# Kernel optimization log

Measured on AMD Instinct MI355X. Metric: run time of the kernel, lower is better.

The kernel has to match this reference:

```python
import jax, jax.numpy as jnp
import numpy as np

N, Cin, H, W = 8, 256, 32, 32
Cout, K = 512, 3
DK, DV, NH = 128, 128, 8
DKH, DVH = DK // NH, DV // NH
HW = H * W


def conv2d(x, w, b, stride, pad):
    y = jax.lax.conv_general_dilated(
        x, w, (stride, stride), [(pad, pad), (pad, pad)],
        dimension_numbers=("NCHW", "OIHW", "NCHW"))
    return y + b[None, :, None, None]


def rel_to_abs(x):
    # x: (B, Nh*, L, 2L-1) -> (B, Nh*, L, L) via pad/reshape trick
    B, Nh, L, _ = x.shape
    x = jnp.concatenate([x, jnp.zeros((B, Nh, L, 1), x.dtype)], axis=3)
    flat = x.reshape(B, Nh, L * 2 * L)
    flat = jnp.concatenate([flat, jnp.zeros((B, Nh, L - 1), x.dtype)], axis=2)
    return flat.reshape(B, Nh, L + 1, 2 * L - 1)[:, :, :L, L - 1:]


def relative_logits_1d(q, rel_k, Hq, Wq, case):
    # q: (N, Nh, Hq, Wq, dkh); rel_k: (2*Wq-1, dkh)
    rl = jnp.einsum('bhxyd,md->bhxym', q, rel_k)             # (N,Nh,Hq,Wq,2Wq-1)
    rl = rel_to_abs(rl.reshape(-1, NH * Hq, Wq, 2 * Wq - 1))  # (N,Nh*Hq,Wq,Wq)
    rl = rl.reshape(-1, NH, Hq, Wq, Wq)[:, :, :, None]        # (N,Nh,Hq,1,Wq,Wq)
    rl = jnp.broadcast_to(rl, (rl.shape[0], NH, Hq, Hq, Wq, Wq))  # axes (b,h,x,i,y,j)
    if case == 'w':
        rl = rl.transpose(0, 1, 2, 4, 3, 5)   # (b,h,x,y,i,j)
    else:  # 'h'
        rl = rl.transpose(0, 1, 4, 2, 5, 3)   # (b,h,y,x,j,i)
    return rl.reshape(-1, NH, HW, HW)


def setup_inputs() -> dict:
    key = jax.random.key(0)
    ks = jax.random.split(key, 9)
    s = 0.05
    return {
        'x': jax.random.normal(ks[0], (N, Cin, H, W), jnp.float32),
        'w_out': jax.random.normal(ks[1], (Cout - DV, Cin, K, K), jnp.float32) * s,
        'b_out': jnp.zeros((Cout - DV,), jnp.float32),
        'w_kqv': jax.random.normal(ks[2], (2 * DK + DV, Cin, 1, 1), jnp.float32) * s,
        'b_kqv': jnp.zeros((2 * DK + DV,), jnp.float32),
        'w_attn': jax.random.normal(ks[3], (DV, DV, 1, 1), jnp.float32) * s,
        'b_attn': jnp.zeros((DV,), jnp.float32),
        'key_rel_w': jax.random.normal(ks[4], (2 * W - 1, DKH), jnp.float32),
        'key_rel_h': jax.random.normal(ks[5], (2 * H - 1, DKH), jnp.float32),
    }


def reference(x, w_out, b_out, w_kqv, b_kqv, w_attn, b_attn, key_rel_w, key_rel_h):
    conv_out = conv2d(x, w_out, b_out, 1, (K - 1) // 2)       # (N, Cout-DV, H, W)
    kqv = conv2d(x, w_kqv, b_kqv, 1, 0)                       # (N, 2DK+DV, H, W)
    k, q, v = jnp.split(kqv, [DK, 2 * DK], axis=1)
    q = q * (DKH ** -0.5)
    q5 = q.reshape(N, NH, DKH, H, W)
    flat_q = q5.reshape(N, NH, DKH, HW)
    flat_k = k.reshape(N, NH, DKH, HW)
    flat_v = v.reshape(N, NH, DVH, HW)
    logits = jnp.einsum('bhdm,bhdn->bhmn', flat_q, flat_k)    # (N,NH,HW,HW)
    qt = q5.transpose(0, 1, 3, 4, 2)                          # (N,NH,H,W,dkh)
    rl_w = relative_logits_1d(qt, key_rel_w, H, W, 'w')
    rl_h = relative_logits_1d(qt.transpose(0, 1, 3, 2, 4), key_rel_h, W, H, 'h')
    logits = logits + rl_h + rl_w
    weights = jax.nn.softmax(logits, axis=-1)
    attn = jnp.einsum('bhmn,bhdn->bhmd', weights, flat_v)     # (N,NH,HW,DVH)
    # faithful to torch: raw reshape (N,NH,HW,DVH)->(N,NH,DVH,H,W)->(N,DV,H,W)
    attn = attn.reshape(N, DV, H, W)
    attn = conv2d(attn, w_attn, b_attn, 1, 0)
    return jnp.concatenate([conv_out, attn], axis=1)
```

## Files before the change

### kernel.cpp

```cpp
#include <hip/hip_runtime.h>
#include <hip/hip_bf16.h>


typedef short v8s __attribute__((ext_vector_type(8)));
typedef float v4f __attribute__((ext_vector_type(4)));

#define WB2_US   0u
#define WK2_US   884736u
#define WA2_US   983040u
#define KRWB_US  999424u
#define KRHB_US  1000448u
#define XC_US    1001472u
#define ART2_US  3368960u

#define KS_US    0u
#define QS_US    1048576u
#define VTS_US   2097152u
#define ART1_US  7340032u

#define QSCALE 0.360673760f
#define SHIFT2 17.3123405f

__device__ __forceinline__ unsigned short f2bs(float f) {
  __hip_bfloat16 h = __float2bfloat16(f);
  return *reinterpret_cast<unsigned short*>(&h);
}

__global__ __launch_bounds__(256) void prep_kernel(
    const float* __restrict__ w_out, const float* __restrict__ w_kqv,
    const float* __restrict__ w_attn, const float* __restrict__ krw,
    const float* __restrict__ krh, unsigned short* __restrict__ ws) {
  int i = blockIdx.x * 256 + threadIdx.x;
  if (i < 884736) {
    int j = i & 7, l = (i >> 3) & 63;
    int r = i >> 9;
    int tap = r % 9; int r2 = r / 9;
    int kc = r2 & 7, nt = (r2 >> 3) & 3, coG = r2 >> 5;
    int co = coG * 64 + nt * 16 + (l & 15);
    int ci = kc * 32 + (l >> 4) * 8 + j;
    ws[WB2_US + i] = f2bs(w_out[(size_t)co * 2304 + ci * 9 + tap]);
  } else if (i < 983040) {
    int o = i - 884736;
    int j = o & 7, l = (o >> 3) & 63, kc = (o >> 9) & 7, nt = (o >> 12) & 3;
    int coG = o >> 14;
    int co = coG * 64 + nt * 16 + (l & 15);
    int ci = kc * 32 + (l >> 4) * 8 + j;
    ws[WK2_US + o] = f2bs(w_kqv[co * 256 + ci]);
  } else if (i < 999424) {
    int o = i - 983040;
    int j = o & 7, l = (o >> 3) & 63, kc = (o >> 9) & 3, nt = (o >> 11) & 3;
    int coG = o >> 13;
    int co = coG * 64 + nt * 16 + (l & 15);
    int ci = kc * 32 + (l >> 4) * 8 + j;
    ws[WA2_US + o] = f2bs(w_attn[co * 128 + ci]);
  } else if (i < 1000448) {
    int j = i - 999424; int c = j >> 4, d = j & 15;
    ws[KRWB_US + j] = (c < 63) ? f2bs(krw[c * 16 + d]) : (unsigned short)0;
  } else if (i < 1001472) {
    int j = i - 1000448; int c = j >> 4, d = j & 15;
    ws[KRHB_US + j] = (c < 63) ? f2bs(krh[c * 16 + d]) : (unsigned short)0;
  }
}

__global__ __launch_bounds__(256) void zero_xc_kernel(unsigned short* __restrict__ xc) {
  int i = blockIdx.x * 256 + threadIdx.x;
  uint4 z = {0u, 0u, 0u, 0u};
  ((uint4*)xc)[i] = z;
}

__global__ __launch_bounds__(256) void xt_kernel(
    const float* __restrict__ x, unsigned short* __restrict__ xc) {
  __shared__ float t[64][65];
  int tid = threadIdx.x; int pl = tid & 63, cg = tid >> 6;
  int pos0 = blockIdx.x * 64, ci0 = blockIdx.y * 64, b = blockIdx.z;
  const float* xb = x + ((size_t)(b * 256 + ci0)) * 1024 + pos0;
#pragma unroll
  for (int i = 0; i < 16; ++i) {
    int ci_l = cg * 16 + i;
    t[ci_l][pl] = xb[(size_t)ci_l * 1024 + pl];
  }
  __syncthreads();
#pragma unroll
  for (int i = 0; i < 16; ++i) {
    int pos_l = cg * 16 + i;
    int pos = pos0 + pos_l;
    int y = (pos >> 5) + 1, xx = (pos & 31) + 1;
    int ci = ci0 + pl;
    xc[((size_t)((b * 8 + (ci >> 5)) * 34 + y) * 34 + xx) * 32 + (ci & 31)] =
        f2bs(t[pl][pos_l]);
  }
}

__global__ __launch_bounds__(256) void kqv_mfma(
    const unsigned short* __restrict__ xc, const unsigned short* __restrict__ wk2,
    const float* __restrict__ bkqv, unsigned short* __restrict__ dq) {
  int tid = threadIdx.x;
  int lane = tid & 63; int il = lane & 15, q = lane >> 4;
  int wv = tid >> 6; int mh = wv >> 1, nh = wv & 1;
  int m0 = blockIdx.x * 64, coG = blockIdx.y;
  int b = m0 >> 10, pos0 = m0 & 1023;
  int row0 = pos0 >> 5;
  v4f acc[2][2];
#pragma unroll
  for (int mi = 0; mi < 2; ++mi)
#pragma unroll
    for (int ni = 0; ni < 2; ++ni) acc[mi][ni] = (v4f){0.f, 0.f, 0.f, 0.f};

  int pix[2];
#pragma unroll
  for (int mi = 0; mi < 2; ++mi)
    pix[mi] = (row0 + mh + 1) * 34 + (mi * 16 + il + 1);
  const unsigned short* bt = wk2 + (size_t)coG * 16384 + lane * 8;
  const unsigned short* at = xc + (size_t)(b * 8) * 36992 + q * 8;

  v8s afS[4][2], bfS[4][2];
#pragma unroll
  for (int p = 0; p < 3; ++p) {
#pragma unroll
    for (int ni = 0; ni < 2; ++ni)
      bfS[p][ni] = *(const v8s*)(bt + ((nh * 2 + ni) * 8 + p) * 512);
#pragma unroll
    for (int mi = 0; mi < 2; ++mi)
      afS[p][mi] = *(const v8s*)(at + (size_t)p * 36992 + pix[mi] * 32);
  }

#pragma unroll
  for (int kc = 0; kc < 8; ++kc) {
    if (kc + 3 < 8) {
      int kn = kc + 3, s = kn & 3;
#pragma unroll
      for (int ni = 0; ni < 2; ++ni)
        bfS[s][ni] = *(const v8s*)(bt + ((nh * 2 + ni) * 8 + kn) * 512);
#pragma unroll
      for (int mi = 0; mi < 2; ++mi)
        afS[s][mi] = *(const v8s*)(at + (size_t)kn * 36992 + pix[mi] * 32);
    }
    int cs = kc & 3;
#pragma unroll
    for (int mi = 0; mi < 2; ++mi)
#pragma unroll
      for (int ni = 0; ni < 2; ++ni)
        acc[mi][ni] = __builtin_amdgcn_mfma_f32_16x16x32_bf16(
            afS[cs][mi], bfS[cs][ni], acc[mi][ni], 0, 0, 0);
  }
  int co0 = coG * 64;
#pragma unroll
  for (int ni = 0; ni < 2; ++ni) {
    int nt = nh * 2 + ni;
    int cob = co0 + nt * 16;
    int co = cob + il;
    float bias = bkqv[co];
    int cls = cob >> 7;
    int h = (cob >> 4) & 7;
    size_t bh = (size_t)(b * 8 + h);
#pragma unroll
    for (int mi = 0; mi < 2; ++mi) {
      int mt = mh * 2 + mi;
      int pos = pos0 + mt * 16 + q * 4;
      v4f a = acc[mi][ni];
#pragma unroll
      for (int r = 0; r < 4; ++r) {
        float v = a[r] + bias;
        int p = pos + r;
        if (cls == 0)      dq[KS_US + bh * 16384 + p * 16 + il] = f2bs(v);
        else if (cls == 1) dq[QS_US + bh * 16384 + p * 16 + il] = f2bs(v * QSCALE);
        else               dq[VTS_US + bh * 16384 + ((p >> 5) * 16 + il) * 32 + (p & 31)] = f2bs(v);
      }
    }
  }
}

__global__ __launch_bounds__(256) void attn_mfma(
    unsigned short* __restrict__ dq, const unsigned short* __restrict__ krwb,
    const unsigned short* __restrict__ krhb, unsigned short* __restrict__ wsart) {
  __shared__ float lds[4][2448];
  int tid = threadIdx.x; int w = tid >> 6, lane = tid & 63;
  int il = lane & 15, q = lane >> 4;
  int bh = blockIdx.y; int b = bh >> 3, h = bh & 7;
  int m0 = blockIdx.x * 64 + w * 16;
  int my = m0 >> 5, mxb = m0 & 31;
  float* pw = lds[w];
  float* ph = pw + 1024;
  unsigned short* pl = (unsigned short*)(ph + 1088);

  const v8s z8 = {0, 0, 0, 0, 0, 0, 0, 0};
  const v4f z4 = {0.f, 0.f, 0.f, 0.f};

  const unsigned short* qrow = dq + QS_US + (size_t)bh * 16384 + (m0 + il) * 16;
  v8s qa = *(const v8s*)(qrow + (q & 1) * 8);
  qa = (q < 2) ? qa : z8;

#pragma unroll
  for (int nt = 0; nt < 4; ++nt) {
    int c = nt * 16 + il;
    v8s bw = *(const v8s*)(krwb + c * 16 + (q & 1) * 8);
    v8s bhh = *(const v8s*)(krhb + c * 16 + (q & 1) * 8);
    bw = (q < 2) ? bw : z8;
    bhh = (q < 2) ? bhh : z8;
    v4f pwc = __builtin_amdgcn_mfma_f32_16x16x32_bf16(qa, bw, z4, 0, 0, 0);
    v4f phc = __builtin_amdgcn_mfma_f32_16x16x32_bf16(qa, bhh, z4, 0, 0, 0);
#pragma unroll
    for (int r = 0; r < 4; ++r) {
      pw[(q * 4 + r) * 64 + c] = pwc[r];
      ph[(q * 4 + r) * 68 + c] = phc[r] - SHIFT2;
    }
  }
  __builtin_amdgcn_wave_barrier();

  float pwv[2][4];
#pragma unroll
  for (int nt2 = 0; nt2 < 2; ++nt2)
#pragma unroll
    for (int r = 0; r < 4; ++r)
      pwv[nt2][r] = pw[il * 64 + (nt2 * 16 + q * 4 + r) - mxb - il + 31];

  v4f oacc = z4;
  float sacc = 0.f;
  const unsigned short* kbase = dq + KS_US + (size_t)bh * 16384;
  const unsigned short* vbase = dq + VTS_US + (size_t)bh * 16384;

  v8s kb0 = *(const v8s*)(kbase + (il) * 16 + (q & 1) * 8);
  v8s kb1 = *(const v8s*)(kbase + (16 + il) * 16 + (q & 1) * 8);
  v8s vb0 = *(const v8s*)(vbase + (il) * 32 + q * 8);

  for (int ny = 0; ny < 32; ++ny) {
    v8s kc0 = (q < 2) ? kb0 : z8;
    v8s kc1 = (q < 2) ? kb1 : z8;
    v8s vcur = vb0;
    if (ny < 31) {
      kb0 = *(const v8s*)(kbase + ((ny + 1) * 32 + il) * 16 + (q & 1) * 8);
      kb1 = *(const v8s*)(kbase + ((ny + 1) * 32 + 16 + il) * 16 + (q & 1) * 8);
      vb0 = *(const v8s*)(vbase + ((ny + 1) * 16 + il) * 32 + q * 8);
    }
    float phv = ph[il * 68 + (ny - my + 31)];
    v4f s[2];
    s[0] = __builtin_amdgcn_mfma_f32_16x16x32_bf16(kc0, qa, z4, 0, 0, 0);
    s[1] = __builtin_amdgcn_mfma_f32_16x16x32_bf16(kc1, qa, z4, 0, 0, 0);
#pragma unroll
    for (int nt2 = 0; nt2 < 2; ++nt2) {
      float p[4];
#pragma unroll
      for (int r = 0; r < 4; ++r) {
        float t = s[nt2][r] + pwv[nt2][r] + phv;
        p[r] = exp2f(t);
        sacc += p[r];
      }
      uint2 pk;
      pk.x = (unsigned)f2bs(p[0]) | ((unsigned)f2bs(p[1]) << 16);
      pk.y = (unsigned)f2bs(p[2]) | ((unsigned)f2bs(p[3]) << 16);
      *(uint2*)(pl + il * 40 + nt2 * 16 + q * 4) = pk;
    }
    __builtin_amdgcn_wave_barrier();
    v8s pf = *(const v8s*)(pl + il * 40 + q * 8);
    oacc = __builtin_amdgcn_mfma_f32_16x16x32_bf16(pf, vcur, oacc, 0, 0, 0);
    __builtin_amdgcn_wave_barrier();
  }

  sacc += __shfl_xor(sacc, 16);
  sacc += __shfl_xor(sacc, 32);

  unsigned short* abase = (b < 6) ? (dq + ART1_US + (size_t)b * 131072)
                                  : (wsart + (size_t)(b - 6) * 131072);
#pragma unroll
  for (int r = 0; r < 4; ++r) {
    float sr = __shfl(sacc, q * 4 + r);
    int m = m0 + q * 4 + r;
    int c = h * 16 + (m >> 6);
    int pp = (m & 63) * 16 + il;
    abase[((c >> 5) * 1024 + pp) * 32 + (c & 31)] = f2bs(oacc[r] / sr);
  }
}

__global__ __launch_bounds__(256) void attn_out_mfma(
    const unsigned short* __restrict__ dq, const unsigned short* __restrict__ wsart,
    const unsigned short* __restrict__ wa2, const float* __restrict__ ba,
    float* __restrict__ out) {
  int tid = threadIdx.x;
  int lane = tid & 63; int il = lane & 15, q = lane >> 4;
  int wv = tid >> 6; int mh = wv >> 1, nh = wv & 1;
  int m0 = blockIdx.x * 64, coG = blockIdx.y;
  int b = m0 >> 10, pp0 = m0 & 1023;
  const unsigned short* ab = (b < 6) ? (dq + ART1_US + (size_t)b * 131072)
                                     : (wsart + (size_t)(b - 6) * 131072);
  const unsigned short* bt = wa2 + (size_t)coG * 8192 + lane * 8;
  v4f acc[2][2];
#pragma unroll
  for (int mi = 0; mi < 2; ++mi)
#pragma unroll
    for (int ni = 0; ni < 2; ++ni) acc[mi][ni] = (v4f){0.f, 0.f, 0.f, 0.f};
#pragma unroll
  for (int kc = 0; kc < 4; ++kc) {
    v8s af[2], bf[2];
#pragma unroll
    for (int ni = 0; ni < 2; ++ni)
      bf[ni] = *(const v8s*)(bt + ((nh * 2 + ni) * 4 + kc) * 512);
#pragma unroll
    for (int mi = 0; mi < 2; ++mi)
      af[mi] = *(const v8s*)(ab + (kc * 1024 + pp0 + (mh * 2 + mi) * 16 + il) * 32 + q * 8);
#pragma unroll
    for (int mi = 0; mi < 2; ++mi)
#pragma unroll
      for (int ni = 0; ni < 2; ++ni)
        acc[mi][ni] = __builtin_amdgcn_mfma_f32_16x16x32_bf16(
            af[mi], bf[ni], acc[mi][ni], 0, 0, 0);
  }
  int co0 = coG * 64;
#pragma unroll
  for (int ni = 0; ni < 2; ++ni) {
    int co = co0 + (nh * 2 + ni) * 16 + il;
    float bias = ba[co];
#pragma unroll
    for (int mi = 0; mi < 2; ++mi) {
      int mt = mh * 2 + mi;
      v4f a = acc[mi][ni];
      float4 v; v.x = a[0] + bias; v.y = a[1] + bias;
      v.z = a[2] + bias; v.w = a[3] + bias;
      *(float4*)(out + ((size_t)(b * 512 + 384 + co)) * 1024 + pp0 + mt * 16 + q * 4) = v;
    }
  }
}

__global__ __launch_bounds__(256, 2) void conv_mfma(
    const unsigned short* __restrict__ xc, const unsigned short* __restrict__ wb3,
    const float* __restrict__ bo, float* __restrict__ out) {
  __shared__ unsigned short xcs[2][4608];
  int tid = threadIdx.x;
  int lane = tid & 63; int il = lane & 15, q = lane >> 4;
  int wv = tid >> 6; int mh = wv >> 1, nh = wv & 1;
  int bx = blockIdx.x, nset = blockIdx.y;
  int b = bx & 7, pt = bx >> 3;
  int pos0 = pt * 64, y0 = pt * 2;
  const unsigned short* xb = xc + ((size_t)(b * 8) * 1156 + y0 * 34) * 32;

  v4f acc[2][3];
#pragma unroll
  for (int mi = 0; mi < 2; ++mi)
#pragma unroll
    for (int j = 0; j < 3; ++j) acc[mi][j] = (v4f){0.f, 0.f, 0.f, 0.f};

  const unsigned short* wp[3];
#pragma unroll
  for (int j = 0; j < 3; ++j) {
    int nfg = nset * 6 + nh * 3 + j;
    int coG = nfg >> 2, nt = nfg & 3;
    wp[j] = wb3 + (size_t)(coG * 4 + nt) * 36864 + lane * 8;
  }

  auto stageX = [&](int buf, int kc) {
    const unsigned short* src = xb + (size_t)kc * 36992;
#pragma unroll
    for (int t = 0; t < 3; ++t) {
      int s = wv + t * 4;
      if (s < 9) {
        int C = s * 64 + lane;
        int row = C / 136, rem = C % 136;
        int qv = rem / 34, xx = rem % 34;
        const unsigned short* g = src + ((row * 136 + xx * 4 + qv) << 3);
        __builtin_amdgcn_global_load_lds(
            (const __attribute__((address_space(1))) void*)g,
            (__attribute__((address_space(3))) void*)(&xcs[buf][s * 512]),
            16, 0, 0);
      }
    }
  };

  stageX(0, 0);
  v8s bS[5][3];
#pragma unroll
  for (int p = 0; p < 4; ++p)
#pragma unroll
    for (int j = 0; j < 3; ++j)
      bS[p][j] = *(const v8s*)(wp[j] + (size_t)p * 512);
  __syncthreads();

#pragma unroll
  for (int kc = 0; kc < 8; ++kc) {
    int buf = kc & 1;
    if (kc < 7) stageX(buf ^ 1, kc + 1);
#pragma unroll
    for (int tap = 0; tap < 9; ++tap) {
      int it = kc * 9 + tap;
      if (it + 4 < 72) {
#pragma unroll
        for (int j = 0; j < 3; ++j)
          bS[(it + 4) % 5][j] = *(const v8s*)(wp[j] + (size_t)(it + 4) * 512);
      }
      int ky = tap / 3, kx = tap % 3;
      v8s af[2];
#pragma unroll
      for (int mi = 0; mi < 2; ++mi)
        af[mi] = *(const v8s*)&xcs[buf][((mh + ky) * 4 + q) * 272 +
                                        (mi * 16 + kx + il) * 8];
#pragma unroll
      for (int mi = 0; mi < 2; ++mi)
#pragma unroll
        for (int j = 0; j < 3; ++j)
          acc[mi][j] = __builtin_amdgcn_mfma_f32_16x16x32_bf16(
              af[mi], bS[it % 5][j], acc[mi][j], 0, 0, 0);
    }
    __syncthreads();
  }

  int co0 = nset * 96;
#pragma unroll
  for (int j = 0; j < 3; ++j) {
    int co = co0 + (nh * 3 + j) * 16 + il;
    float bias = bo[co];
#pragma unroll
    for (int mi = 0; mi < 2; ++mi) {
      v4f a = acc[mi][j];
      float4 v; v.x = a[0] + bias; v.y = a[1] + bias;
      v.z = a[2] + bias; v.w = a[3] + bias;
      *(float4*)(out + ((size_t)(b * 512 + co)) * 1024 +
                 pos0 + mh * 32 + mi * 16 + q * 4) = v;
    }
  }
}

extern "C" void kernel_launch(void* const* d_in, const int* in_sizes, int n_in,
                              void* d_out, int out_size, void* d_ws, size_t ws_size,
                              hipStream_t stream) {
  const float* x      = (const float*)d_in[0];
  const float* b_out  = (const float*)d_in[2];
  const float* b_kqv  = (const float*)d_in[4];
  const float* b_attn = (const float*)d_in[6];
  const float* krw    = (const float*)d_in[7];
  const float* krh    = (const float*)d_in[8];
  unsigned short* ws = (unsigned short*)d_ws;
  float* out = (float*)d_out;
  unsigned short* dq = (unsigned short*)d_out;

  prep_kernel<<<3912, 256, 0, stream>>>(
      (const float*)d_in[1], (const float*)d_in[3], (const float*)d_in[5],
      krw, krh, ws);
  zero_xc_kernel<<<1156, 256, 0, stream>>>(ws + XC_US);
  xt_kernel<<<dim3(16, 4, 8), 256, 0, stream>>>(x, ws + XC_US);
  kqv_mfma<<<dim3(128, 6), 256, 0, stream>>>(
      ws + XC_US, ws + WK2_US, b_kqv, dq);
  attn_mfma<<<dim3(16, 64), 256, 0, stream>>>(
      dq, ws + KRWB_US, ws + KRHB_US, ws + ART2_US);
  attn_out_mfma<<<dim3(128, 2), 256, 0, stream>>>(
      dq, ws + ART2_US, ws + WA2_US, b_attn, out);
  conv_mfma<<<dim3(128, 4), 256, 0, stream>>>(
      ws + XC_US, ws + WB2_US, b_out, out);
}
```

Measured before the change: 159.3 us.

## Stage conv weights in LDS and double block tile to 512 threads

The 3x3 conv kernel now uses 512-thread blocks covering four image rows instead of two, halving the grid. Weight fragments are loaded into LDS once per channel chunk and shared by all eight waves, where previously each wave streamed its own weights from global memory into registers. The X and weight tiles are single-buffered: loads happen between two barriers after each chunk's MFMAs, so the previous overlap of the next chunk's loads with compute is lost. LDS use grows to about 68 KB per block.

```diff
diff --git a/kernel.cpp b/kernel.cpp
--- a/kernel.cpp
+++ b/kernel.cpp
@@ -320,16 +320,17 @@
   }
 }
 
-__global__ __launch_bounds__(256, 2) void conv_mfma(
+__global__ __launch_bounds__(512, 4) void conv_mfma(
     const unsigned short* __restrict__ xc, const unsigned short* __restrict__ wb3,
     const float* __restrict__ bo, float* __restrict__ out) {
-  __shared__ unsigned short xcs[2][4608];
+  __shared__ unsigned short xlds[6656];
+  __shared__ unsigned short wlds[27648];
   int tid = threadIdx.x;
   int lane = tid & 63; int il = lane & 15, q = lane >> 4;
   int wv = tid >> 6; int mh = wv >> 1, nh = wv & 1;
   int bx = blockIdx.x, nset = blockIdx.y;
   int b = bx & 7, pt = bx >> 3;
-  int pos0 = pt * 64, y0 = pt * 2;
+  int pos0 = pt * 128, y0 = pt * 4;
   const unsigned short* xb = xc + ((size_t)(b * 8) * 1156 + y0 * 34) * 32;
 
   v4f acc[2][3];
@@ -338,67 +339,71 @@
 #pragma unroll
     for (int j = 0; j < 3; ++j) acc[mi][j] = (v4f){0.f, 0.f, 0.f, 0.f};
 
-  const unsigned short* wp[3];
-#pragma unroll
-  for (int j = 0; j < 3; ++j) {
-    int nfg = nset * 6 + nh * 3 + j;
-    int coG = nfg >> 2, nt = nfg & 3;
-    wp[j] = wb3 + (size_t)(coG * 4 + nt) * 36864 + lane * 8;
-  }
-
-  auto stageX = [&](int buf, int kc) {
+  auto stageX = [&](int kc) {
     const unsigned short* src = xb + (size_t)kc * 36992;
 #pragma unroll
-    for (int t = 0; t < 3; ++t) {
-      int s = wv + t * 4;
-      if (s < 9) {
-        int C = s * 64 + lane;
-        int row = C / 136, rem = C % 136;
+    for (int t = 0; t < 2; ++t) {
+      int s = wv + t * 8;
+      if (s < 13) {
+        int c = s * 64 + lane;
+        int row = c / 136, rem = c % 136;
         int qv = rem / 34, xx = rem % 34;
         const unsigned short* g = src + ((row * 136 + xx * 4 + qv) << 3);
         __builtin_amdgcn_global_load_lds(
             (const __attribute__((address_space(1))) void*)g,
-            (__attribute__((address_space(3))) void*)(&xcs[buf][s * 512]),
+            (__attribute__((address_space(3))) void*)(&xlds[s * 512]),
             16, 0, 0);
       }
     }
   };
 
-  stageX(0, 0);
-  v8s bS[5][3];
-#pragma unroll
-  for (int p = 0; p < 4; ++p)
-#pragma unroll
-    for (int j = 0; j < 3; ++j)
-      bS[p][j] = *(const v8s*)(wp[j] + (size_t)p * 512);
+  auto stageW = [&](int kc) {
+#pragma unroll
+    for (int t = 0; t < 7; ++t) {
+      int s = wv + t * 8;
+      if (s < 54) {
+        int nfg = s / 9, tp = s % 9;
+        const unsigned short* g = wb3 +
+            ((size_t)(((nset * 6 + nfg) * 8 + kc) * 9 + tp) * 512 + lane * 8);
+        __builtin_amdgcn_global_load_lds(
+            (const __attribute__((address_space(1))) void*)g,
+            (__attribute__((address_space(3))) void*)(&wlds[s * 512]),
+            16, 0, 0);
+      }
+    }
+  };
+
+  stageX(0);
+  stageW(0);
   __syncthreads();
 
-#pragma unroll
   for (int kc = 0; kc < 8; ++kc) {
-    int buf = kc & 1;
-    if (kc < 7) stageX(buf ^ 1, kc + 1);
 #pragma unroll
     for (int tap = 0; tap < 9; ++tap) {
-      int it = kc * 9 + tap;
-      if (it + 4 < 72) {
-#pragma unroll
-        for (int j = 0; j < 3; ++j)
-          bS[(it + 4) % 5][j] = *(const v8s*)(wp[j] + (size_t)(it + 4) * 512);
+      int ky = tap / 3, kx = tap % 3;
+      v8s af[2], bf[3];
+#pragma unroll
+      for (int j = 0; j < 3; ++j)
+        bf[j] = *(const v8s*)&wlds[((nh * 3 + j) * 9 + tap) * 512 + lane * 8];
+#pragma unroll
+      for (int mi = 0; mi < 2; ++mi) {
+        int mf = mh * 2 + mi;
+        af[mi] = *(const v8s*)&xlds[((((mf >> 1) + ky) * 4 + q) * 34 +
+                                     ((mf & 1) * 16 + kx + il)) * 8];
       }
-      int ky = tap / 3, kx = tap % 3;
-      v8s af[2];
-#pragma unroll
-      for (int mi = 0; mi < 2; ++mi)
-        af[mi] = *(const v8s*)&xcs[buf][((mh + ky) * 4 + q) * 272 +
-                                        (mi * 16 + kx + il) * 8];
 #pragma unroll
       for (int mi = 0; mi < 2; ++mi)
 #pragma unroll
         for (int j = 0; j < 3; ++j)
           acc[mi][j] = __builtin_amdgcn_mfma_f32_16x16x32_bf16(
-              af[mi], bS[it % 5][j], acc[mi][j], 0, 0, 0);
-    }
-    __syncthreads();
+              af[mi], bf[j], acc[mi][j], 0, 0, 0);
+    }
+    if (kc < 7) {
+      __syncthreads();
+      stageX(kc + 1);
+      stageW(kc + 1);
+      __syncthreads();
+    }
   }
 
   int co0 = nset * 96;
@@ -408,11 +413,12 @@
     float bias = bo[co];
 #pragma unroll
     for (int mi = 0; mi < 2; ++mi) {
+      int mf = mh * 2 + mi;
       v4f a = acc[mi][j];
       float4 v; v.x = a[0] + bias; v.y = a[1] + bias;
       v.z = a[2] + bias; v.w = a[3] + bias;
       *(float4*)(out + ((size_t)(b * 512 + co)) * 1024 +
-                 pos0 + mh * 32 + mi * 16 + q * 4) = v;
+                 pos0 + mf * 16 + q * 4) = v;
     }
   }
 }
@@ -441,6 +447,6 @@
       dq, ws + KRWB_US, ws + KRHB_US, ws + ART2_US);
   attn_out_mfma<<<dim3(128, 2), 256, 0, stream>>>(
       dq, ws + ART2_US, ws + WA2_US, b_attn, out);
-  conv_mfma<<<dim3(128, 4), 256, 0, stream>>>(
+  conv_mfma<<<dim3(64, 4), 512, 0, stream>>>(
       ws + XC_US, ws + WB2_US, b_out, out);
 }
```

Result: faster. 154.6 us (-2.9%).
